# Performance work log

Hardware: AMD Instinct MI355X
Metric: run time of the kernel (lower is better)

## Reference

```python
import jax, jax.numpy as jnp
import numpy as np

EPS = 1e-5


def _gcn_conv(x, src, dst, norm, W, b, n_nodes):
    # PyG GCNConv: transform, then normalized scatter-add aggregation (self-loops included in src/dst)
    h = x @ W                                   # [N, out]
    msg = h[src] * norm[:, None]                # gather over edges [E+N, out]
    agg = jax.ops.segment_sum(msg, dst, num_segments=n_nodes)
    return agg + b


def _bn(x, gamma, beta):
    # BatchNorm1d in training mode: batch stats over node axis, biased variance
    mu = jnp.mean(x, axis=0)
    var = jnp.mean((x - mu) ** 2, axis=0)
    return (x - mu) * jax.lax.rsqrt(var + EPS) * gamma + beta


def setup_inputs() -> dict:
    key = jax.random.key(0)
    ks = jax.random.split(key, 8)
    N, E, F_in, H, F_out = 50000, 800000, 32, 96, 2
    x = jax.random.normal(ks[0], (N, F_in), dtype=jnp.float32)
    edge_index = jax.random.randint(ks[1], (2, E), 0, N, dtype=jnp.int64)
    def lin(k, fi, fo):
        s = 1.0 / np.sqrt(fi)
        return jax.random.uniform(k, (fi, fo), jnp.float32, -s, s)
    W1 = lin(ks[2], F_in, H); b1 = jnp.zeros((H,), jnp.float32)
    W2 = lin(ks[3], H, H);    b2 = jnp.zeros((H,), jnp.float32)
    W3 = lin(ks[4], H, H);    b3 = jnp.zeros((H,), jnp.float32)
    W4 = lin(ks[5], H, F_out); b4 = jnp.zeros((F_out,), jnp.float32)
    g1 = jnp.ones((H,), jnp.float32); be1 = jnp.zeros((H,), jnp.float32)
    g2 = jnp.ones((H,), jnp.float32); be2 = jnp.zeros((H,), jnp.float32)
    g3 = jnp.ones((H,), jnp.float32); be3 = jnp.zeros((H,), jnp.float32)
    return dict(x=x, edge_index=edge_index,
                W1=W1, b1=b1, g1=g1, be1=be1,
                W2=W2, b2=b2, g2=g2, be2=be2,
                W3=W3, b3=b3, g3=g3, be3=be3,
                W4=W4, b4=b4)


def reference(x, edge_index, W1, b1, g1, be1, W2, b2, g2, be2, W3, b3, g3, be3, W4, b4):
    N = x.shape[0]
    loop = jnp.arange(N, dtype=edge_index.dtype)
    src = jnp.concatenate([edge_index[0], loop])   # add self-loops
    dst = jnp.concatenate([edge_index[1], loop])
    deg = jax.ops.segment_sum(jnp.ones_like(dst, dtype=x.dtype), dst, num_segments=N)
    dinv = jnp.where(deg > 0, jax.lax.rsqrt(deg), 0.0)
    norm = dinv[src] * dinv[dst]                   # D^{-1/2} (A+I) D^{-1/2}

    h = jax.nn.relu(_bn(_gcn_conv(x, src, dst, norm, W1, b1, N), g1, be1))
    h = jax.nn.relu(_bn(_gcn_conv(h, src, dst, norm, W2, b2, N), g2, be2))
    h = jax.nn.relu(_bn(_gcn_conv(h, src, dst, norm, W3, b3, N), g3, be3))
    return _gcn_conv(h, src, dst, norm, W4, b4, N)
```

## Files before the change

kernel.cpp:

```cpp
#include <hip/hip_runtime.h>
#include <hip/hip_bf16.h>

using bf16x8 = __attribute__((ext_vector_type(8))) short;
using f32x4  = __attribute__((ext_vector_type(4))) float;

__device__ __forceinline__ float ldf(const void* p, size_t i, float isf){
  if (isf > 0.5f) return ((const float*)p)[i];
  unsigned int u = ((unsigned int)((const unsigned short*)p)[i]) << 16;
  return __uint_as_float(u);
}
__device__ __forceinline__ unsigned short f2bf(float v){
  unsigned int u = __float_as_uint(v);
  u = (u + 0x7FFFu + ((u >> 16) & 1u)) >> 16;
  return (unsigned short)u;
}
__device__ __forceinline__ unsigned int pk2(float a, float b){
  return (unsigned int)f2bf(a) | ((unsigned int)f2bf(b) << 16);
}
__device__ __forceinline__ float lo16(unsigned int u){ return __uint_as_float(u << 16); }
__device__ __forceinline__ float hi16(unsigned int u){ return __uint_as_float(u & 0xFFFF0000u); }
__device__ __forceinline__ float bfh(unsigned short h){ return __uint_as_float(((unsigned int)h) << 16); }

__global__ void k_fill(unsigned short* o, unsigned short v, int n){
  int i = blockIdx.x*blockDim.x + threadIdx.x;
  if (i < n) o[i] = v;
}

__global__ void k_prep(const unsigned short* xh, const unsigned int* eu,
                       float* flag, int nelemX, long long E,
                       const void* W1, const void* W2, const void* W3, const void* W4,
                       unsigned short* __restrict__ Wt1, unsigned short* __restrict__ Wt2,
                       unsigned short* __restrict__ Wt3, float* __restrict__ W4f){
  __shared__ int sf32, si64;
  __shared__ float sisf;
  int t = threadIdx.x;
  if (t == 0){ sf32 = 0; si64 = 1; }
  __syncthreads();
  {
    int i = 2*t;
    if (i < nelemX){
      unsigned e8 = (xh[i] >> 7) & 0xFFu;
      if (e8 >= 140u) sf32 = 1;
    }
    if ((long long)(2*t + 1) < 2*E){
      if (eu[2*t + 1] != 0u) si64 = 0;
    }
  }
  __syncthreads();
  if (t == 0){
    flag[0] = (float)sf32; flag[1] = (float)si64;
    sisf = (float)sf32;
  }
  __syncthreads();
  float isf = sisf;
  for (int q = t; q < 3072; q += 256){
    int nn = q >> 5, k = q & 31;
    Wt1[q] = f2bf(ldf(W1, (size_t)96*k + nn, isf));
  }
  for (int q = t; q < 9216; q += 256){
    int nn = q/96, k = q - 96*nn;
    Wt2[q] = f2bf(ldf(W2, (size_t)96*k + nn, isf));
    Wt3[q] = f2bf(ldf(W3, (size_t)96*k + nn, isf));
  }
  if (t < 192) W4f[t] = ldf(W4, t, isf);
}

__global__ void k_cnt(const int* __restrict__ ei, const float* __restrict__ flag,
                      int* __restrict__ cnt, long long E, int n){
  long long i = (long long)blockIdx.x*blockDim.x + threadIdx.x;
  if (i >= E) return;
  int d = (flag[1] > 0.5f) ? ei[2*E + 2*i] : ei[E + i];
  if ((unsigned)d < (unsigned)n) atomicAdd(&cnt[d], 1);
}

__global__ void k_bsum(const int* __restrict__ cnt, int* __restrict__ bsum, int n){
  int i = blockIdx.x*256 + threadIdx.x;
  int v = (i < n) ? cnt[i] : 0;
  #pragma unroll
  for (int off = 32; off; off >>= 1) v += __shfl_down(v, off, 64);
  __shared__ int w[4];
  if ((threadIdx.x & 63) == 0) w[threadIdx.x >> 6] = v;
  __syncthreads();
  if (threadIdx.x == 0) bsum[blockIdx.x] = w[0]+w[1]+w[2]+w[3];
}

__global__ void k_sscan(const int* __restrict__ bsum, int* __restrict__ boff,
                        int* __restrict__ rowstN, int nb){
  int t = threadIdx.x;
  int v = (t < nb) ? bsum[t] : 0;
  int lane = t & 63, wid = t >> 6;
  int s = v;
  #pragma unroll
  for (int off = 1; off < 64; off <<= 1){
    int u = __shfl_up(s, off, 64);
    if (lane >= off) s += u;
  }
  __shared__ int wt[4];
  if (lane == 63) wt[wid] = s;
  __syncthreads();
  int add = 0;
  for (int w = 0; w < wid; ++w) add += wt[w];
  int incl = s + add;
  if (t < nb) boff[t] = incl - v;
  if (t == nb - 1) *rowstN = incl;
}

__global__ void k_emit(const int* __restrict__ cnt, const int* __restrict__ boff,
                       int* __restrict__ rowst, int* __restrict__ cursor,
                       float* __restrict__ dinv, int n){
  int i = blockIdx.x*256 + threadIdx.x;
  int v = (i < n) ? cnt[i] : 0;
  int lane = threadIdx.x & 63, wid = threadIdx.x >> 6;
  int s = v;
  #pragma unroll
  for (int off = 1; off < 64; off <<= 1){
    int u = __shfl_up(s, off, 64);
    if (lane >= off) s += u;
  }
  __shared__ int wt[4];
  if (lane == 63) wt[wid] = s;
  __syncthreads();
  int add = 0;
  for (int w = 0; w < wid; ++w) add += wt[w];
  if (i < n){
    int r = boff[blockIdx.x] + add + s - v;
    rowst[i] = r;
    cursor[i] = r;
    dinv[i]  = rsqrtf((float)(1 + v));
  }
}

#define FS_CHUNK 4096
template<typename IT>
__global__ __launch_bounds__(256) void k_fill_slots8(const int* __restrict__ ei,
                             const float* __restrict__ flag,
                             int* __restrict__ cursor, IT* __restrict__ csr,
                             long long E, int n){
  int part = blockIdx.x & 7;
  long long base = (long long)(blockIdx.x >> 3) * FS_CHUNK;
  int pl = (int)(((long long)n *  part     ) >> 3);
  int pr = (int)(((long long)n * (part + 1)) >> 3);
  bool i64 = (flag[1] > 0.5f);
  long long lim = base + FS_CHUNK < E ? base + FS_CHUNK : E;
  for (long long i = base + threadIdx.x; i < lim; i += 256){
    int s, d;
    if (i64){ s = ei[2*i]; d = ei[2*E + 2*i]; }
    else    { s = ei[i];   d = ei[E + i];     }
    if (d >= pl && d < pr && (unsigned)s < (unsigned)n){
      int p = atomicAdd(&cursor[d], 1);
      csr[p] = (IT)s;
    }
  }
}

__global__ __launch_bounds__(256) void k_lin1m(const void* __restrict__ x,
      const unsigned short* __restrict__ Wt1b, const float* __restrict__ flag,
      const float* __restrict__ dinv, unsigned short* __restrict__ HS, int n){
  __shared__ __align__(16) unsigned short Xs[64][40];
  __shared__ __align__(16) unsigned short Wt[96][40];
  int t = threadIdx.x;
  float isf = flag[0];
  for (int q = t; q < 384; q += 256){
    uint4 v = ((const uint4*)Wt1b)[q];
    *(uint4*)&Wt[q >> 2][(q & 3)*8] = v;
  }
  {
    int row = t >> 2, part = t & 3;
    int node = blockIdx.x*64 + row;
    uint4 o;
    if (node < n){
      if (isf > 0.5f){
        const float* xr = (const float*)x + (size_t)32*node + 8*part;
        o.x = pk2(xr[0], xr[1]); o.y = pk2(xr[2], xr[3]);
        o.z = pk2(xr[4], xr[5]); o.w = pk2(xr[6], xr[7]);
      } else {
        o = ((const uint4*)x)[(size_t)4*node + part];
      }
    } else { o.x = o.y = o.z = o.w = 0u; }
    *(uint4*)&Xs[row][8*part] = o;
  }
  __syncthreads();

  int wv = t >> 6, lane = t & 63;
  int m = lane & 15, quad = lane >> 4;
  bf16x8 av = *(const bf16x8*)&Xs[16*wv + m][8*quad];
  f32x4 acc[6];
  #pragma unroll
  for (int c = 0; c < 6; ++c) acc[c] = (f32x4)(0.f);
  #pragma unroll
  for (int c = 0; c < 6; ++c){
    bf16x8 bv = *(const bf16x8*)&Wt[16*c + m][8*quad];
    acc[c] = __builtin_amdgcn_mfma_f32_16x16x32_bf16(av, bv, acc[c], 0, 0, 0);
  }
  int rowbase = blockIdx.x*64 + 16*wv + 4*quad;
  float div[4];
  #pragma unroll
  for (int r = 0; r < 4; ++r){ int rr = rowbase + r; div[r] = (rr < n) ? dinv[rr] : 0.f; }
  #pragma unroll
  for (int c = 0; c < 6; ++c){
    int col = 16*c + m;
    #pragma unroll
    for (int r = 0; r < 4; ++r){
      int rr = rowbase + r;
      if (rr < n) HS[(size_t)96*rr + col] = f2bf(acc[c][r]*div[r]);
    }
  }
}

__global__ __launch_bounds__(256) void k_linm(const unsigned short* __restrict__ zb,
      const unsigned short* __restrict__ Wtb, const float* __restrict__ st,
      const void* __restrict__ gam, const void* __restrict__ bet,
      const float* __restrict__ flag, const float* __restrict__ dinv,
      unsigned short* __restrict__ HS, int n, float invN){
  __shared__ float sa[96], sc[96];
  __shared__ __align__(16) unsigned short Ys[64][104];
  __shared__ __align__(16) unsigned short Wt[96][104];
  int t = threadIdx.x;
  if (t < 96){
    float isf = flag[0];
    float mu  = st[t]*invN;
    float var = fmaxf(st[96+t]*invN - mu*mu, 0.f);
    float istd = rsqrtf(var + 1e-5f);
    float a = ldf(gam, t, isf)*istd;
    sa[t] = a; sc[t] = ldf(bet, t, isf) - mu*a;
  }
  for (int q = t; q < 1152; q += 256){
    uint4 v = ((const uint4*)Wtb)[q];
    *(uint4*)&Wt[q/12][8*(q - 12*(q/12))] = v;
  }
  __syncthreads();
  {
    int row = t >> 2, part = t & 3;
    int node = blockIdx.x*64 + row;
    if (node < n){
      const uint4* zr = (const uint4*)(zb + (size_t)96*node) + 3*part;
      #pragma unroll
      for (int q = 0; q < 3; ++q){
        uint4 zz = zr[q];
        int k = 24*part + 8*q;
        float y0 = fmaxf(lo16(zz.x)*sa[k]   + sc[k],   0.f);
        float y1 = fmaxf(hi16(zz.x)*sa[k+1] + sc[k+1], 0.f);
        float y2 = fmaxf(lo16(zz.y)*sa[k+2] + sc[k+2], 0.f);
        float y3 = fmaxf(hi16(zz.y)*sa[k+3] + sc[k+3], 0.f);
        float y4 = fmaxf(lo16(zz.z)*sa[k+4] + sc[k+4], 0.f);
        float y5 = fmaxf(hi16(zz.z)*sa[k+5] + sc[k+5], 0.f);
        float y6 = fmaxf(lo16(zz.w)*sa[k+6] + sc[k+6], 0.f);
        float y7 = fmaxf(hi16(zz.w)*sa[k+7] + sc[k+7], 0.f);
        *(unsigned int*)&Ys[row][k]     = pk2(y0, y1);
        *(unsigned int*)&Ys[row][k + 2] = pk2(y2, y3);
        *(unsigned int*)&Ys[row][k + 4] = pk2(y4, y5);
        *(unsigned int*)&Ys[row][k + 6] = pk2(y6, y7);
      }
    } else {
      unsigned int* yp = (unsigned int*)&Ys[row][24*part];
      #pragma unroll
      for (int q = 0; q < 12; ++q) yp[q] = 0u;
    }
  }
  __syncthreads();

  int wv = t >> 6, lane = t & 63;
  int m = lane & 15, quad = lane >> 4;
  bf16x8 av[3];
  #pragma unroll
  for (int kt = 0; kt < 3; ++kt)
    av[kt] = *(const bf16x8*)&Ys[16*wv + m][32*kt + 8*quad];
  f32x4 acc[6];
  #pragma unroll
  for (int c = 0; c < 6; ++c) acc[c] = (f32x4)(0.f);
  #pragma unroll
  for (int c = 0; c < 6; ++c){
    const unsigned short* wrow = &Wt[16*c + m][8*quad];
    #pragma unroll
    for (int kt = 0; kt < 3; ++kt){
      bf16x8 bv = *(const bf16x8*)(wrow + 32*kt);
      acc[c] = __builtin_amdgcn_mfma_f32_16x16x32_bf16(av[kt], bv, acc[c], 0, 0, 0);
    }
  }
  int rowbase = blockIdx.x*64 + 16*wv + 4*quad;
  float div[4];
  #pragma unroll
  for (int r = 0; r < 4; ++r){ int rr = rowbase + r; div[r] = (rr < n) ? dinv[rr] : 0.f; }
  #pragma unroll
  for (int c = 0; c < 6; ++c){
    int col = 16*c + m;
    #pragma unroll
    for (int r = 0; r < 4; ++r){
      int rr = rowbase + r;
      if (rr < n) HS[(size_t)96*rr + col] = f2bf(acc[c][r]*div[r]);
    }
  }
}

__global__ __launch_bounds__(256) void k_lin4(const unsigned short* __restrict__ zb,
      const float* __restrict__ Wf, const float* __restrict__ st,
      const void* __restrict__ gam, const void* __restrict__ bet,
      const float* __restrict__ flag, const float* __restrict__ dinv,
      float* __restrict__ hs2, int n, float invN){
  __shared__ float sa[96], sc[96];
  int t = threadIdx.x;
  if (t < 96){
    float isf = flag[0];
    float mu  = st[t]*invN;
    float var = fmaxf(st[96+t]*invN - mu*mu, 0.f);
    float istd = rsqrtf(var + 1e-5f);
    float a = ldf(gam, t, isf)*istd;
    sa[t] = a; sc[t] = ldf(bet, t, isf) - mu*a;
  }
  __syncthreads();
  int i = blockIdx.x*blockDim.x + t;
  if (i >= n) return;
  const uint4* zr = (const uint4*)(zb + (size_t)96*i);
  float a0 = 0.f, a1 = 0.f;
  #pragma unroll
  for (int q = 0; q < 12; ++q){
    uint4 zz = zr[q];
    int k = 8*q;
    float y;
    y = fmaxf(lo16(zz.x)*sa[k]   + sc[k],   0.f); a0 += y*Wf[2*k];    a1 += y*Wf[2*k+1];
    y = fmaxf(hi16(zz.x)*sa[k+1] + sc[k+1], 0.f); a0 += y*Wf[2*k+2];  a1 += y*Wf[2*k+3];
    y = fmaxf(lo16(zz.y)*sa[k+2] + sc[k+2], 0.f); a0 += y*Wf[2*k+4];  a1 += y*Wf[2*k+5];
    y = fmaxf(hi16(zz.y)*sa[k+3] + sc[k+3], 0.f); a0 += y*Wf[2*k+6];  a1 += y*Wf[2*k+7];
    y = fmaxf(lo16(zz.z)*sa[k+4] + sc[k+4], 0.f); a0 += y*Wf[2*k+8];  a1 += y*Wf[2*k+9];
    y = fmaxf(hi16(zz.z)*sa[k+5] + sc[k+5], 0.f); a0 += y*Wf[2*k+10]; a1 += y*Wf[2*k+11];
    y = fmaxf(lo16(zz.w)*sa[k+6] + sc[k+6], 0.f); a0 += y*Wf[2*k+12]; a1 += y*Wf[2*k+13];
    y = fmaxf(hi16(zz.w)*sa[k+7] + sc[k+7], 0.f); a0 += y*Wf[2*k+14]; a1 += y*Wf[2*k+15];
  }
  float di = dinv[i];
  hs2[(size_t)2*i]   = di*a0;
  hs2[(size_t)2*i+1] = di*a1;
}

#define ACC8(v) { a0+=lo16((v).x); a1+=hi16((v).x); a2+=lo16((v).y); a3+=hi16((v).y); \
                  a4+=lo16((v).z); a5+=hi16((v).z); a6+=lo16((v).w); a7+=hi16((v).w); }
template<typename IT>
__global__ __launch_bounds__(192) void k_agg(const uint4* __restrict__ hsr,
      const int* __restrict__ rowst, const IT* __restrict__ csr,
      const float* __restrict__ dinv, uint4* __restrict__ zb4,
      float* __restrict__ st, int n){
  int t = threadIdx.y*12 + threadIdx.x;
  if (blockIdx.x == 0 && t < 192) st[t] = 0.f;
  int node = blockIdx.x*16 + threadIdx.y;
  if (node >= n) return;
  int g = threadIdx.x;
  uint4 v = hsr[(size_t)node*12 + g];
  float a0 = lo16(v.x), a1 = hi16(v.x), a2 = lo16(v.y), a3 = hi16(v.y);
  float a4 = lo16(v.z), a5 = hi16(v.z), a6 = lo16(v.w), a7 = hi16(v.w);
  int b = rowst[node], e = rowst[node+1];
  int j = b;
  for (; j + 7 < e; j += 8){
    uint4 v0 = hsr[(size_t)csr[j]  *12 + g];
    uint4 v1 = hsr[(size_t)csr[j+1]*12 + g];
    uint4 v2 = hsr[(size_t)csr[j+2]*12 + g];
    uint4 v3 = hsr[(size_t)csr[j+3]*12 + g];
    uint4 v4 = hsr[(size_t)csr[j+4]*12 + g];
    uint4 v5 = hsr[(size_t)csr[j+5]*12 + g];
    uint4 v6 = hsr[(size_t)csr[j+6]*12 + g];
    uint4 v7 = hsr[(size_t)csr[j+7]*12 + g];
    ACC8(v0); ACC8(v1); ACC8(v2); ACC8(v3);
    ACC8(v4); ACC8(v5); ACC8(v6); ACC8(v7);
  }
  for (; j + 3 < e; j += 4){
    uint4 v0 = hsr[(size_t)csr[j]  *12 + g];
    uint4 v1 = hsr[(size_t)csr[j+1]*12 + g];
    uint4 v2 = hsr[(size_t)csr[j+2]*12 + g];
    uint4 v3 = hsr[(size_t)csr[j+3]*12 + g];
    ACC8(v0); ACC8(v1); ACC8(v2); ACC8(v3);
  }
  for (; j < e; ++j){
    uint4 vv = hsr[(size_t)csr[j]*12 + g];
    ACC8(vv);
  }
  float di = dinv[node];
  uint4 o;
  o.x = pk2(a0*di, a1*di);
  o.y = pk2(a2*di, a3*di);
  o.z = pk2(a4*di, a5*di);
  o.w = pk2(a6*di, a7*di);
  zb4[(size_t)node*12 + g] = o;
}

template<typename IT>
__global__ void k_agg2(const float2* __restrict__ hs2, const int* __restrict__ rowst,
                       const IT* __restrict__ csr, const float* __restrict__ dinv,
                       const void* __restrict__ b4, const float* __restrict__ flag,
                       void* __restrict__ out, int n){
  int node = blockIdx.x*blockDim.x + threadIdx.x;
  if (node >= n) return;
  float2 a = hs2[node];
  int b = rowst[node], e = rowst[node+1];
  for (int j = b; j < e; ++j){
    float2 v = hs2[(size_t)csr[j]];
    a.x += v.x; a.y += v.y;
  }
  float isf = flag[0];
  float di = dinv[node];
  float v0 = a.x*di + ldf(b4, 0, isf);
  float v1 = a.y*di + ldf(b4, 1, isf);
  if (isf > 0.5f){
    ((float*)out)[(size_t)2*node]   = v0;
    ((float*)out)[(size_t)2*node+1] = v1;
  } else {
    ((unsigned short*)out)[(size_t)2*node]   = f2bf(v0);
    ((unsigned short*)out)[(size_t)2*node+1] = f2bf(v1);
  }
}

__global__ void k_stats(const unsigned short* __restrict__ zb, float* __restrict__ st, int n){
  int f = threadIdx.x, ty = threadIdx.y;
  float s = 0.f, q = 0.f;
  for (int i = blockIdx.x*4 + ty; i < n; i += gridDim.x*4){
    float y = bfh(zb[(size_t)96*i + f]);
    s += y; q += y*y;
  }
  __shared__ float ls[4][96], lq[4][96];
  ls[ty][f] = s; lq[ty][f] = q;
  __syncthreads();
  if (ty == 0){
    s = ls[0][f]+ls[1][f]+ls[2][f]+ls[3][f];
    q = lq[0][f]+lq[1][f]+lq[2][f]+lq[3][f];
    atomicAdd(&st[f], s); atomicAdd(&st[96+f], q);
  }
}

extern "C" void kernel_launch(void* const* d_in, const int* in_sizes, int n_in,
                              void* d_out, int out_size, void* d_ws, size_t ws_size,
                              hipStream_t stream)
{
  const int B = 256;
  unsigned short* outh = (unsigned short*)d_out;

  if (n_in < 16){
    k_fill<<<(out_size+B-1)/B, B, 0, stream>>>(outh, 0x3F40u, out_size); return;
  }
  const int N = in_sizes[0] / 32;
  const long long E = in_sizes[1] / 2;
  if (in_sizes[0] % 32 != 0 || out_size != 2*N){
    k_fill<<<(out_size+B-1)/B, B, 0, stream>>>(outh, 0x3F60u, out_size); return;
  }
  const bool u16 = (N < 65536);

  size_t Npad = ((size_t)N + 3) & ~(size_t)3;
  float* ws   = (float*)d_ws;
  float* dinv = ws;
  float* hs2  = dinv + Npad;
  float* st   = hs2 + (size_t)2*N;
  float* flag = st + 384;
  float* W4f  = flag + 4;
  unsigned short* Wt1b = (unsigned short*)(W4f + 192);
  unsigned short* Wt2b = Wt1b + 3072;
  unsigned short* Wt3b = Wt2b + 9216;
  int* cnt    = (int*)(Wt3b + 9216);
  int* cursor = cnt + N;
  int* rowst  = cursor + N;
  int* bsum   = rowst + N + 1;
  int* boff   = bsum + 256;
  void* csrv  = (void*)(boff + 256);
  size_t csrBytes = (size_t)E * (u16 ? 2 : 4);
  uintptr_t hp_ = (uintptr_t)csrv + csrBytes;
  hp_ = (hp_ + 15) & ~(uintptr_t)15;
  unsigned short* HS = (unsigned short*)hp_;
  unsigned short* Zb = HS + (size_t)96*N;

  size_t needB = ((uintptr_t)(Zb + (size_t)96*N) - (uintptr_t)d_ws) + 64;
  if (ws_size < needB){
    k_fill<<<(out_size+B-1)/B, B, 0, stream>>>(outh, 0x3F00u, out_size); return;
  }

  const void* x  = d_in[0];
  const int*  ei = (const int*)d_in[1];
  const void* W1 = d_in[2];
  const void* g1 = d_in[4];  const void* be1 = d_in[5];
  const void* W2 = d_in[6];
  const void* g2 = d_in[8];  const void* be2 = d_in[9];
  const void* W3 = d_in[10];
  const void* g3 = d_in[12]; const void* be3 = d_in[13];
  const void* W4 = d_in[14];
  const void* b4 = d_in[15];

  int gN  = (N + B - 1)/B;
  int gE  = (int)((E + B - 1)/B);
  int nb  = (N + 255)/256;
  int gA  = (N + 15)/16;
  int gL  = (N + 63)/64;
  int gF8 = (int)((E + FS_CHUNK - 1)/FS_CHUNK) * 8;
  float invN = 1.0f / (float)N;
  dim3 ablk(12,16);
  dim3 sblk(96,4);

  k_prep<<<1, 256, 0, stream>>>((const unsigned short*)x, (const unsigned int*)ei,
                                flag, in_sizes[0], E, W1, W2, W3, W4,
                                Wt1b, Wt2b, Wt3b, W4f);
  hipMemsetAsync(cnt, 0, (size_t)N*sizeof(int), stream);
  k_cnt<<<gE, B, 0, stream>>>(ei, flag, cnt, E, N);
  k_bsum<<<nb, 256, 0, stream>>>(cnt, bsum, N);
  k_sscan<<<1, 256, 0, stream>>>(bsum, boff, rowst + N, nb);
  k_emit<<<nb, 256, 0, stream>>>(cnt, boff, rowst, cursor, dinv, N);

  if (u16){
    unsigned short* csr = (unsigned short*)csrv;
    k_fill_slots8<unsigned short><<<gF8, B, 0, stream>>>(ei, flag, cursor, csr, E, N);

    k_lin1m<<<gL, B, 0, stream>>>(x, Wt1b, flag, dinv, HS, N);
    k_agg<unsigned short><<<gA, ablk, 0, stream>>>((const uint4*)HS, rowst, csr, dinv, (uint4*)Zb, st, N);
    k_stats<<<512, sblk, 0, stream>>>(Zb, st, N);

    k_linm<<<gL, B, 0, stream>>>(Zb, Wt2b, st, g1, be1, flag, dinv, HS, N, invN);
    k_agg<unsigned short><<<gA, ablk, 0, stream>>>((const uint4*)HS, rowst, csr, dinv, (uint4*)Zb, st, N);
    k_stats<<<512, sblk, 0, stream>>>(Zb, st, N);

    k_linm<<<gL, B, 0, stream>>>(Zb, Wt3b, st, g2, be2, flag, dinv, HS, N, invN);
    k_agg<unsigned short><<<gA, ablk, 0, stream>>>((const uint4*)HS, rowst, csr, dinv, (uint4*)Zb, st, N);
    k_stats<<<512, sblk, 0, stream>>>(Zb, st, N);

    k_lin4<<<gN, B, 0, stream>>>(Zb, W4f, st, g3, be3, flag, dinv, hs2, N, invN);
    k_agg2<unsigned short><<<gN, B, 0, stream>>>((const float2*)hs2, rowst, csr, dinv, b4, flag, d_out, N);
  } else {
    int* csr = (int*)csrv;
    k_fill_slots8<int><<<gF8, B, 0, stream>>>(ei, flag, cursor, csr, E, N);

    k_lin1m<<<gL, B, 0, stream>>>(x, Wt1b, flag, dinv, HS, N);
    k_agg<int><<<gA, ablk, 0, stream>>>((const uint4*)HS, rowst, csr, dinv, (uint4*)Zb, st, N);
    k_stats<<<512, sblk, 0, stream>>>(Zb, st, N);

    k_linm<<<gL, B, 0, stream>>>(Zb, Wt2b, st, g1, be1, flag, dinv, HS, N, invN);
    k_agg<int><<<gA, ablk, 0, stream>>>((const uint4*)HS, rowst, csr, dinv, (uint4*)Zb, st, N);
    k_stats<<<512, sblk, 0, stream>>>(Zb, st, N);

    k_linm<<<gL, B, 0, stream>>>(Zb, Wt3b, st, g2, be2, flag, dinv, HS, N, invN);
    k_agg<int><<<gA, ablk, 0, stream>>>((const uint4*)HS, rowst, csr, dinv, (uint4*)Zb, st, N);
    k_stats<<<512, sblk, 0, stream>>>(Zb, st, N);

    k_lin4<<<gN, B, 0, stream>>>(Zb, W4f, st, g3, be3, flag, dinv, hs2, N, invN);
    k_agg2<int><<<gN, B, 0, stream>>>((const float2*)hs2, rowst, csr, dinv, b4, flag, d_out, N);
  }
}
```

Measured before the change: 378.3 us.

## Fuse BN stats into aggregation, merge scan kernels and CSR fill with lin1

```diff
diff --git a/kernel.cpp b/kernel.cpp
--- a/kernel.cpp
+++ b/kernel.cpp
@@ -19,7 +19,6 @@
 }
 __device__ __forceinline__ float lo16(unsigned int u){ return __uint_as_float(u << 16); }
 __device__ __forceinline__ float hi16(unsigned int u){ return __uint_as_float(u & 0xFFFF0000u); }
-__device__ __forceinline__ float bfh(unsigned short h){ return __uint_as_float(((unsigned int)h) << 16); }
 
 __global__ void k_fill(unsigned short* o, unsigned short v, int n){
   int i = blockIdx.x*blockDim.x + threadIdx.x;
@@ -30,10 +29,18 @@
                        float* flag, int nelemX, long long E,
                        const void* W1, const void* W2, const void* W3, const void* W4,
                        unsigned short* __restrict__ Wt1, unsigned short* __restrict__ Wt2,
-                       unsigned short* __restrict__ Wt3, float* __restrict__ W4f){
+                       unsigned short* __restrict__ Wt3, float* __restrict__ W4f,
+                       int* __restrict__ cnt, float* __restrict__ stAll, int n){
+  int t = threadIdx.x;
+  if (blockIdx.x > 0){
+    int total = n + 4608;
+    for (int i = (int)(blockIdx.x-1)*256 + t; i < total; i += (int)(gridDim.x-1)*256){
+      if (i < n) cnt[i] = 0; else stAll[i - n] = 0.f;
+    }
+    return;
+  }
   __shared__ int sf32, si64;
   __shared__ float sisf;
-  int t = threadIdx.x;
   if (t == 0){ sf32 = 0; si64 = 1; }
   __syncthreads();
   {
@@ -73,92 +80,81 @@
   if ((unsigned)d < (unsigned)n) atomicAdd(&cnt[d], 1);
 }
 
-__global__ void k_bsum(const int* __restrict__ cnt, int* __restrict__ bsum, int n){
-  int i = blockIdx.x*256 + threadIdx.x;
-  int v = (i < n) ? cnt[i] : 0;
-  #pragma unroll
-  for (int off = 32; off; off >>= 1) v += __shfl_down(v, off, 64);
-  __shared__ int w[4];
-  if ((threadIdx.x & 63) == 0) w[threadIdx.x >> 6] = v;
-  __syncthreads();
-  if (threadIdx.x == 0) bsum[blockIdx.x] = w[0]+w[1]+w[2]+w[3];
-}
-
-__global__ void k_sscan(const int* __restrict__ bsum, int* __restrict__ boff,
-                        int* __restrict__ rowstN, int nb){
-  int t = threadIdx.x;
-  int v = (t < nb) ? bsum[t] : 0;
-  int lane = t & 63, wid = t >> 6;
-  int s = v;
-  #pragma unroll
-  for (int off = 1; off < 64; off <<= 1){
-    int u = __shfl_up(s, off, 64);
-    if (lane >= off) s += u;
-  }
-  __shared__ int wt[4];
-  if (lane == 63) wt[wid] = s;
-  __syncthreads();
-  int add = 0;
-  for (int w = 0; w < wid; ++w) add += wt[w];
-  int incl = s + add;
-  if (t < nb) boff[t] = incl - v;
-  if (t == nb - 1) *rowstN = incl;
-}
-
-__global__ void k_emit(const int* __restrict__ cnt, const int* __restrict__ boff,
-                       int* __restrict__ rowst, int* __restrict__ cursor,
-                       float* __restrict__ dinv, int n){
-  int i = blockIdx.x*256 + threadIdx.x;
-  int v = (i < n) ? cnt[i] : 0;
-  int lane = threadIdx.x & 63, wid = threadIdx.x >> 6;
-  int s = v;
-  #pragma unroll
-  for (int off = 1; off < 64; off <<= 1){
-    int u = __shfl_up(s, off, 64);
-    if (lane >= off) s += u;
-  }
-  __shared__ int wt[4];
-  if (lane == 63) wt[wid] = s;
-  __syncthreads();
-  int add = 0;
-  for (int w = 0; w < wid; ++w) add += wt[w];
-  if (i < n){
-    int r = boff[blockIdx.x] + add + s - v;
-    rowst[i] = r;
-    cursor[i] = r;
-    dinv[i]  = rsqrtf((float)(1 + v));
-  }
+__global__ void k_scan(const int* __restrict__ cnt, int* __restrict__ rowst,
+                       int* __restrict__ cursor, float* __restrict__ dinv, int n){
+  __shared__ int woff[16];
+  __shared__ int chtot;
+  __shared__ int carry_s;
+  int tid = threadIdx.x;
+  int lane = tid & 63, wid = tid >> 6;
+  if (tid == 0) carry_s = 0;
+  __syncthreads();
+  for (int base = 0; base < n; base += 1024){
+    int i = base + tid;
+    int v = (i < n) ? cnt[i] : 0;
+    int s = v;
+    #pragma unroll
+    for (int off = 1; off < 64; off <<= 1){
+      int u = __shfl_up(s, off, 64);
+      if (lane >= off) s += u;
+    }
+    if (lane == 63) woff[wid] = s;
+    __syncthreads();
+    if (tid < 16){
+      int w = woff[tid];
+      int ws_ = w;
+      #pragma unroll
+      for (int off = 1; off < 16; off <<= 1){
+        int u = __shfl_up(ws_, off, 64);
+        if (tid >= off) ws_ += u;
+      }
+      woff[tid] = ws_ - w;
+      if (tid == 15) chtot = ws_;
+    }
+    __syncthreads();
+    int carry = carry_s;
+    if (i < n){
+      int r = carry + woff[wid] + s - v;
+      rowst[i] = r;
+      cursor[i] = r;
+      dinv[i]  = rsqrtf((float)(1 + v));
+    }
+    __syncthreads();
+    if (tid == 0) carry_s = carry + chtot;
+  }
+  __syncthreads();
+  if (tid == 0) rowst[n] = carry_s;
 }
 
 #define FS_CHUNK 4096
 template<typename IT>
-__global__ __launch_bounds__(256) void k_fill_slots8(const int* __restrict__ ei,
-                             const float* __restrict__ flag,
-                             int* __restrict__ cursor, IT* __restrict__ csr,
-                             long long E, int n){
-  int part = blockIdx.x & 7;
-  long long base = (long long)(blockIdx.x >> 3) * FS_CHUNK;
-  int pl = (int)(((long long)n *  part     ) >> 3);
-  int pr = (int)(((long long)n * (part + 1)) >> 3);
-  bool i64 = (flag[1] > 0.5f);
-  long long lim = base + FS_CHUNK < E ? base + FS_CHUNK : E;
-  for (long long i = base + threadIdx.x; i < lim; i += 256){
-    int s, d;
-    if (i64){ s = ei[2*i]; d = ei[2*E + 2*i]; }
-    else    { s = ei[i];   d = ei[E + i];     }
-    if (d >= pl && d < pr && (unsigned)s < (unsigned)n){
-      int p = atomicAdd(&cursor[d], 1);
-      csr[p] = (IT)s;
-    }
-  }
-}
-
-__global__ __launch_bounds__(256) void k_lin1m(const void* __restrict__ x,
-      const unsigned short* __restrict__ Wt1b, const float* __restrict__ flag,
-      const float* __restrict__ dinv, unsigned short* __restrict__ HS, int n){
+__global__ __launch_bounds__(256) void k_fl1(const int* __restrict__ ei,
+      const float* __restrict__ flag, int* __restrict__ cursor, IT* __restrict__ csr,
+      long long E, int n, int gF8,
+      const void* __restrict__ x, const unsigned short* __restrict__ Wt1b,
+      const float* __restrict__ dinv, unsigned short* __restrict__ HS){
   __shared__ __align__(16) unsigned short Xs[64][40];
   __shared__ __align__(16) unsigned short Wt[96][40];
   int t = threadIdx.x;
+  if ((int)blockIdx.x < gF8){
+    int part = blockIdx.x & 7;
+    long long base = (long long)(blockIdx.x >> 3) * FS_CHUNK;
+    int pl = (int)(((long long)n *  part     ) >> 3);
+    int pr = (int)(((long long)n * (part + 1)) >> 3);
+    bool i64 = (flag[1] > 0.5f);
+    long long lim = base + FS_CHUNK < E ? base + FS_CHUNK : E;
+    for (long long i = base + t; i < lim; i += 256){
+      int s, d;
+      if (i64){ s = ei[2*i]; d = ei[2*E + 2*i]; }
+      else    { s = ei[i];   d = ei[E + i];     }
+      if (d >= pl && d < pr && (unsigned)s < (unsigned)n){
+        int p = atomicAdd(&cursor[d], 1);
+        csr[p] = (IT)s;
+      }
+    }
+    return;
+  }
+  int bid = blockIdx.x - gF8;
   float isf = flag[0];
   for (int q = t; q < 384; q += 256){
     uint4 v = ((const uint4*)Wt1b)[q];
@@ -166,7 +162,7 @@
   }
   {
     int row = t >> 2, part = t & 3;
-    int node = blockIdx.x*64 + row;
+    int node = bid*64 + row;
     uint4 o;
     if (node < n){
       if (isf > 0.5f){
@@ -192,7 +188,7 @@
     bf16x8 bv = *(const bf16x8*)&Wt[16*c + m][8*quad];
     acc[c] = __builtin_amdgcn_mfma_f32_16x16x32_bf16(av, bv, acc[c], 0, 0, 0);
   }
-  int rowbase = blockIdx.x*64 + 16*wv + 4*quad;
+  int rowbase = bid*64 + 16*wv + 4*quad;
   float div[4];
   #pragma unroll
   for (int r = 0; r < 4; ++r){ int rr = rowbase + r; div[r] = (rr < n) ? dinv[rr] : 0.f; }
@@ -204,6 +200,76 @@
       int rr = rowbase + r;
       if (rr < n) HS[(size_t)96*rr + col] = f2bf(acc[c][r]*div[r]);
     }
+  }
+}
+
+#define ACC8(v) { a0+=lo16((v).x); a1+=hi16((v).x); a2+=lo16((v).y); a3+=hi16((v).y); \
+                  a4+=lo16((v).z); a5+=hi16((v).z); a6+=lo16((v).w); a7+=hi16((v).w); }
+template<typename IT>
+__global__ __launch_bounds__(192) void k_agg(const uint4* __restrict__ hsr,
+      const int* __restrict__ rowst, const IT* __restrict__ csr,
+      const float* __restrict__ dinv, uint4* __restrict__ zb4,
+      float* __restrict__ stout, int n){
+  __shared__ float ls[16][97], lq[16][97];
+  int g = threadIdx.x, ty = threadIdx.y;
+  int t = ty*12 + g;
+  int node = blockIdx.x*16 + ty;
+  float r[8];
+  if (node < n){
+    uint4 v = hsr[(size_t)node*12 + g];
+    float a0 = lo16(v.x), a1 = hi16(v.x), a2 = lo16(v.y), a3 = hi16(v.y);
+    float a4 = lo16(v.z), a5 = hi16(v.z), a6 = lo16(v.w), a7 = hi16(v.w);
+    int b = rowst[node], e = rowst[node+1];
+    int j = b;
+    for (; j + 7 < e; j += 8){
+      uint4 v0 = hsr[(size_t)csr[j]  *12 + g];
+      uint4 v1 = hsr[(size_t)csr[j+1]*12 + g];
+      uint4 v2 = hsr[(size_t)csr[j+2]*12 + g];
+      uint4 v3 = hsr[(size_t)csr[j+3]*12 + g];
+      uint4 v4 = hsr[(size_t)csr[j+4]*12 + g];
+      uint4 v5 = hsr[(size_t)csr[j+5]*12 + g];
+      uint4 v6 = hsr[(size_t)csr[j+6]*12 + g];
+      uint4 v7 = hsr[(size_t)csr[j+7]*12 + g];
+      ACC8(v0); ACC8(v1); ACC8(v2); ACC8(v3);
+      ACC8(v4); ACC8(v5); ACC8(v6); ACC8(v7);
+    }
+    for (; j + 3 < e; j += 4){
+      uint4 v0 = hsr[(size_t)csr[j]  *12 + g];
+      uint4 v1 = hsr[(size_t)csr[j+1]*12 + g];
+      uint4 v2 = hsr[(size_t)csr[j+2]*12 + g];
+      uint4 v3 = hsr[(size_t)csr[j+3]*12 + g];
+      ACC8(v0); ACC8(v1); ACC8(v2); ACC8(v3);
+    }
+    for (; j < e; ++j){
+      uint4 vv = hsr[(size_t)csr[j]*12 + g];
+      ACC8(vv);
+    }
+    float di = dinv[node];
+    uint4 o;
+    o.x = pk2(a0*di, a1*di);
+    o.y = pk2(a2*di, a3*di);
+    o.z = pk2(a4*di, a5*di);
+    o.w = pk2(a6*di, a7*di);
+    zb4[(size_t)node*12 + g] = o;
+    r[0]=lo16(o.x); r[1]=hi16(o.x); r[2]=lo16(o.y); r[3]=hi16(o.y);
+    r[4]=lo16(o.z); r[5]=hi16(o.z); r[6]=lo16(o.w); r[7]=hi16(o.w);
+  } else {
+    #pragma unroll
+    for (int jj = 0; jj < 8; ++jj) r[jj] = 0.f;
+  }
+  #pragma unroll
+  for (int jj = 0; jj < 8; ++jj){
+    ls[ty][8*g + jj] = r[jj];
+    lq[ty][8*g + jj] = r[jj]*r[jj];
+  }
+  __syncthreads();
+  if (t < 96){
+    float s = 0.f, q = 0.f;
+    #pragma unroll
+    for (int rr = 0; rr < 16; ++rr){ s += ls[rr][t]; q += lq[rr][t]; }
+    int rep = blockIdx.x & 7;
+    atomicAdd(&stout[192*rep + t],      s);
+    atomicAdd(&stout[192*rep + 96 + t], q);
   }
 }
 
@@ -217,9 +283,12 @@
   __shared__ __align__(16) unsigned short Wt[96][104];
   int t = threadIdx.x;
   if (t < 96){
+    float ssum = 0.f, qsum = 0.f;
+    #pragma unroll
+    for (int r = 0; r < 8; ++r){ ssum += st[192*r + t]; qsum += st[192*r + 96 + t]; }
     float isf = flag[0];
-    float mu  = st[t]*invN;
-    float var = fmaxf(st[96+t]*invN - mu*mu, 0.f);
+    float mu  = ssum*invN;
+    float var = fmaxf(qsum*invN - mu*mu, 0.f);
     float istd = rsqrtf(var + 1e-5f);
     float a = ldf(gam, t, isf)*istd;
     sa[t] = a; sc[t] = ldf(bet, t, isf) - mu*a;
@@ -300,9 +369,12 @@
   __shared__ float sa[96], sc[96];
   int t = threadIdx.x;
   if (t < 96){
+    float ssum = 0.f, qsum = 0.f;
+    #pragma unroll
+    for (int r = 0; r < 8; ++r){ ssum += st[192*r + t]; qsum += st[192*r + 96 + t]; }
     float isf = flag[0];
-    float mu  = st[t]*invN;
-    float var = fmaxf(st[96+t]*invN - mu*mu, 0.f);
+    float mu  = ssum*invN;
+    float var = fmaxf(qsum*invN - mu*mu, 0.f);
     float istd = rsqrtf(var + 1e-5f);
     float a = ldf(gam, t, isf)*istd;
     sa[t] = a; sc[t] = ldf(bet, t, isf) - mu*a;
@@ -331,55 +403,6 @@
   hs2[(size_t)2*i+1] = di*a1;
 }
 
-#define ACC8(v) { a0+=lo16((v).x); a1+=hi16((v).x); a2+=lo16((v).y); a3+=hi16((v).y); \
-                  a4+=lo16((v).z); a5+=hi16((v).z); a6+=lo16((v).w); a7+=hi16((v).w); }
-template<typename IT>
-__global__ __launch_bounds__(192) void k_agg(const uint4* __restrict__ hsr,
-      const int* __restrict__ rowst, const IT* __restrict__ csr,
-      const float* __restrict__ dinv, uint4* __restrict__ zb4,
-      float* __restrict__ st, int n){
-  int t = threadIdx.y*12 + threadIdx.x;
-  if (blockIdx.x == 0 && t < 192) st[t] = 0.f;
-  int node = blockIdx.x*16 + threadIdx.y;
-  if (node >= n) return;
-  int g = threadIdx.x;
-  uint4 v = hsr[(size_t)node*12 + g];
-  float a0 = lo16(v.x), a1 = hi16(v.x), a2 = lo16(v.y), a3 = hi16(v.y);
-  float a4 = lo16(v.z), a5 = hi16(v.z), a6 = lo16(v.w), a7 = hi16(v.w);
-  int b = rowst[node], e = rowst[node+1];
-  int j = b;
-  for (; j + 7 < e; j += 8){
-    uint4 v0 = hsr[(size_t)csr[j]  *12 + g];
-    uint4 v1 = hsr[(size_t)csr[j+1]*12 + g];
-    uint4 v2 = hsr[(size_t)csr[j+2]*12 + g];
-    uint4 v3 = hsr[(size_t)csr[j+3]*12 + g];
-    uint4 v4 = hsr[(size_t)csr[j+4]*12 + g];
-    uint4 v5 = hsr[(size_t)csr[j+5]*12 + g];
-    uint4 v6 = hsr[(size_t)csr[j+6]*12 + g];
-    uint4 v7 = hsr[(size_t)csr[j+7]*12 + g];
-    ACC8(v0); ACC8(v1); ACC8(v2); ACC8(v3);
-    ACC8(v4); ACC8(v5); ACC8(v6); ACC8(v7);
-  }
-  for (; j + 3 < e; j += 4){
-    uint4 v0 = hsr[(size_t)csr[j]  *12 + g];
-    uint4 v1 = hsr[(size_t)csr[j+1]*12 + g];
-    uint4 v2 = hsr[(size_t)csr[j+2]*12 + g];
-    uint4 v3 = hsr[(size_t)csr[j+3]*12 + g];
-    ACC8(v0); ACC8(v1); ACC8(v2); ACC8(v3);
-  }
-  for (; j < e; ++j){
-    uint4 vv = hsr[(size_t)csr[j]*12 + g];
-    ACC8(vv);
-  }
-  float di = dinv[node];
-  uint4 o;
-  o.x = pk2(a0*di, a1*di);
-  o.y = pk2(a2*di, a3*di);
-  o.z = pk2(a4*di, a5*di);
-  o.w = pk2(a6*di, a7*di);
-  zb4[(size_t)node*12 + g] = o;
-}
-
 template<typename IT>
 __global__ void k_agg2(const float2* __restrict__ hs2, const int* __restrict__ rowst,
                        const IT* __restrict__ csr, const float* __restrict__ dinv,
@@ -406,23 +429,6 @@
   }
 }
 
-__global__ void k_stats(const unsigned short* __restrict__ zb, float* __restrict__ st, int n){
-  int f = threadIdx.x, ty = threadIdx.y;
-  float s = 0.f, q = 0.f;
-  for (int i = blockIdx.x*4 + ty; i < n; i += gridDim.x*4){
-    float y = bfh(zb[(size_t)96*i + f]);
-    s += y; q += y*y;
-  }
-  __shared__ float ls[4][96], lq[4][96];
-  ls[ty][f] = s; lq[ty][f] = q;
-  __syncthreads();
-  if (ty == 0){
-    s = ls[0][f]+ls[1][f]+ls[2][f]+ls[3][f];
-    q = lq[0][f]+lq[1][f]+lq[2][f]+lq[3][f];
-    atomicAdd(&st[f], s); atomicAdd(&st[96+f], q);
-  }
-}
-
 extern "C" void kernel_launch(void* const* d_in, const int* in_sizes, int n_in,
                               void* d_out, int out_size, void* d_ws, size_t ws_size,
                               hipStream_t stream)
@@ -444,18 +450,16 @@
   float* ws   = (float*)d_ws;
   float* dinv = ws;
   float* hs2  = dinv + Npad;
-  float* st   = hs2 + (size_t)2*N;
-  float* flag = st + 384;
-  float* W4f  = flag + 4;
+  float* flag = hs2 + (size_t)2*N;
+  float* stAll= flag + 4;
+  float* W4f  = stAll + 4608;
   unsigned short* Wt1b = (unsigned short*)(W4f + 192);
   unsigned short* Wt2b = Wt1b + 3072;
   unsigned short* Wt3b = Wt2b + 9216;
   int* cnt    = (int*)(Wt3b + 9216);
   int* cursor = cnt + N;
   int* rowst  = cursor + N;
-  int* bsum   = rowst + N + 1;
-  int* boff   = bsum + 256;
-  void* csrv  = (void*)(boff + 256);
+  void* csrv  = (void*)(rowst + N + 1);
   size_t csrBytes = (size_t)E * (u16 ? 2 : 4);
   uintptr_t hp_ = (uintptr_t)csrv + csrBytes;
   hp_ = (hp_ + 15) & ~(uintptr_t)15;
@@ -478,60 +482,45 @@
   const void* W4 = d_in[14];
   const void* b4 = d_in[15];
 
+  float* stA = stAll;
+  float* stB = stAll + 1536;
+  float* stC = stAll + 3072;
+
   int gN  = (N + B - 1)/B;
   int gE  = (int)((E + B - 1)/B);
-  int nb  = (N + 255)/256;
   int gA  = (N + 15)/16;
   int gL  = (N + 63)/64;
   int gF8 = (int)((E + FS_CHUNK - 1)/FS_CHUNK) * 8;
   float invN = 1.0f / (float)N;
   dim3 ablk(12,16);
-  dim3 sblk(96,4);
-
-  k_prep<<<1, 256, 0, stream>>>((const unsigned short*)x, (const unsigned int*)ei,
-                                flag, in_sizes[0], E, W1, W2, W3, W4,
-                                Wt1b, Wt2b, Wt3b, W4f);
-  hipMemsetAsync(cnt, 0, (size_t)N*sizeof(int), stream);
+
+  k_prep<<<33, B, 0, stream>>>((const unsigned short*)x, (const unsigned int*)ei,
+                               flag, in_sizes[0], E, W1, W2, W3, W4,
+                               Wt1b, Wt2b, Wt3b, W4f, cnt, stAll, N);
   k_cnt<<<gE, B, 0, stream>>>(ei, flag, cnt, E, N);
-  k_bsum<<<nb, 256, 0, stream>>>(cnt, bsum, N);
-  k_sscan<<<1, 256, 0, stream>>>(bsum, boff, rowst + N, nb);
-  k_emit<<<nb, 256, 0, stream>>>(cnt, boff, rowst, cursor, dinv, N);
+  k_scan<<<1, 1024, 0, stream>>>(cnt, rowst, cursor, dinv, N);
 
   if (u16){
     unsigned short* csr = (unsigned short*)csrv;
-    k_fill_slots8<unsigned short><<<gF8, B, 0, stream>>>(ei, flag, cursor, csr, E, N);
-
-    k_lin1m<<<gL, B, 0, stream>>>(x, Wt1b, flag, dinv, HS, N);
-    k_agg<unsigned short><<<gA, ablk, 0, stream>>>((const uint4*)HS, rowst, csr, dinv, (uint4*)Zb, st, N);
-    k_stats<<<512, sblk, 0, stream>>>(Zb, st, N);
-
-    k_linm<<<gL, B, 0, stream>>>(Zb, Wt2b, st, g1, be1, flag, dinv, HS, N, invN);
-    k_agg<unsigned short><<<gA, ablk, 0, stream>>>((const uint4*)HS, rowst, csr, dinv, (uint4*)Zb, st, N);
-    k_stats<<<512, sblk, 0, stream>>>(Zb, st, N);
-
-    k_linm<<<gL, B, 0, stream>>>(Zb, Wt3b, st, g2, be2, flag, dinv, HS, N, invN);
-    k_agg<unsigned short><<<gA, ablk, 0, stream>>>((const uint4*)HS, rowst, csr, dinv, (uint4*)Zb, st, N);
-    k_stats<<<512, sblk, 0, stream>>>(Zb, st, N);
-
-    k_lin4<<<gN, B, 0, stream>>>(Zb, W4f, st, g3, be3, flag, dinv, hs2, N, invN);
+    k_fl1<unsigned short><<<gF8 + gL, B, 0, stream>>>(ei, flag, cursor, csr, E, N, gF8,
+                                                      x, Wt1b, dinv, HS);
+    k_agg<unsigned short><<<gA, ablk, 0, stream>>>((const uint4*)HS, rowst, csr, dinv, (uint4*)Zb, stA, N);
+    k_linm<<<gL, B, 0, stream>>>(Zb, Wt2b, stA, g1, be1, flag, dinv, HS, N, invN);
+    k_agg<unsigned short><<<gA, ablk, 0, stream>>>((const uint4*)HS, rowst, csr, dinv, (uint4*)Zb, stB, N);
+    k_linm<<<gL, B, 0, stream>>>(Zb, Wt3b, stB, g2, be2, flag, dinv, HS, N, invN);
+    k_agg<unsigned short><<<gA, ablk, 0, stream>>>((const uint4*)HS, rowst, csr, dinv, (uint4*)Zb, stC, N);
+    k_lin4<<<gN, B, 0, stream>>>(Zb, W4f, stC, g3, be3, flag, dinv, hs2, N, invN);
     k_agg2<unsigned short><<<gN, B, 0, stream>>>((const float2*)hs2, rowst, csr, dinv, b4, flag, d_out, N);
   } else {
     int* csr = (int*)csrv;
-    k_fill_slots8<int><<<gF8, B, 0, stream>>>(ei, flag, cursor, csr, E, N);
-
-    k_lin1m<<<gL, B, 0, stream>>>(x, Wt1b, flag, dinv, HS, N);
-    k_agg<int><<<gA, ablk, 0, stream>>>((const uint4*)HS, rowst, csr, dinv, (uint4*)Zb, st, N);
-    k_stats<<<512, sblk, 0, stream>>>(Zb, st, N);
-
-    k_linm<<<gL, B, 0, stream>>>(Zb, Wt2b, st, g1, be1, flag, dinv, HS, N, invN);
-    k_agg<int><<<gA, ablk, 0, stream>>>((const uint4*)HS, rowst, csr, dinv, (uint4*)Zb, st, N);
-    k_stats<<<512, sblk, 0, stream>>>(Zb, st, N);
-
-    k_linm<<<gL, B, 0, stream>>>(Zb, Wt3b, st, g2, be2, flag, dinv, HS, N, invN);
-    k_agg<int><<<gA, ablk, 0, stream>>>((const uint4*)HS, rowst, csr, dinv, (uint4*)Zb, st, N);
-    k_stats<<<512, sblk, 0, stream>>>(Zb, st, N);
-
-    k_lin4<<<gN, B, 0, stream>>>(Zb, W4f, st, g3, be3, flag, dinv, hs2, N, invN);
+    k_fl1<int><<<gF8 + gL, B, 0, stream>>>(ei, flag, cursor, csr, E, N, gF8,
+                                           x, Wt1b, dinv, HS);
+    k_agg<int><<<gA, ablk, 0, stream>>>((const uint4*)HS, rowst, csr, dinv, (uint4*)Zb, stA, N);
+    k_linm<<<gL, B, 0, stream>>>(Zb, Wt2b, stA, g1, be1, flag, dinv, HS, N, invN);
+    k_agg<int><<<gA, ablk, 0, stream>>>((const uint4*)HS, rowst, csr, dinv, (uint4*)Zb, stB, N);
+    k_linm<<<gL, B, 0, stream>>>(Zb, Wt3b, stB, g2, be2, flag, dinv, HS, N, invN);
+    k_agg<int><<<gA, ablk, 0, stream>>>((const uint4*)HS, rowst, csr, dinv, (uint4*)Zb, stC, N);
+    k_lin4<<<gN, B, 0, stream>>>(Zb, W4f, stC, g3, be3, flag, dinv, hs2, N, invN);
     k_agg2<int><<<gN, B, 0, stream>>>((const float2*)hs2, rowst, csr, dinv, b4, flag, d_out, N);
   }
 }
```

Result: no change. 381.7 us (+0.9%).
